# Kernel tuning notes

Measured on AMD Instinct MI355X. Metric: run time of the kernel, lower is better.

## Reference

```python
import jax, jax.numpy as jnp
import numpy as np

N = 50000  # nodes
E = 1600000  # edges
L = 2  # layers
D = 128  # input/hidden dim


def setup_inputs() -> dict:
    key = jax.random.key(0)
    ks = jax.random.split(key, 8)
    s = 1.0 / np.sqrt(D)
    return {
        "x": jax.random.normal(ks[0], (N, D), jnp.float32),
        "edge_index": jax.random.randint(ks[1], (2, E), 0, N, jnp.int64),
        "h": jax.random.normal(ks[2], (L, N, D), jnp.float32),
        "Wx": jax.random.normal(ks[3], (L, 3, D, D), jnp.float32) * s,
        "bx": jax.random.normal(ks[4], (L, 3, D), jnp.float32) * 0.01,
        "Wh": jax.random.normal(ks[5], (L, 3, D, D), jnp.float32) * s,
        "bh": jax.random.normal(ks[6], (L, 3, D), jnp.float32) * 0.01,
    }


def _gcn(x, W, b, src, dst, dinv):
    # GCNConv with added self-loops and symmetric normalization:
    # out = D^{-1/2} (A + I) D^{-1/2} X W + b
    hw = x @ W                                   # [N, H]
    norm = dinv[src] * dinv[dst]                 # [E]
    msg = hw[src] * norm[:, None]                # [E, H]
    agg = jax.ops.segment_sum(msg, dst, num_segments=N)
    agg = agg + hw * (dinv * dinv)[:, None]      # self-loop contribution
    return agg + b


def reference(x, edge_index, h, Wx, bx, Wh, bh):
    src = edge_index[0]
    dst = edge_index[1]
    # in-degree on destination nodes, including self-loop (+1)
    deg = jax.ops.segment_sum(jnp.ones((E,), x.dtype), dst, num_segments=N) + 1.0
    dinv = jax.lax.rsqrt(deg)

    outs = []
    inp = x
    for l in range(L):
        hl = h[l]
        z = jax.nn.sigmoid(_gcn(inp, Wx[l, 0], bx[l, 0], src, dst, dinv)
                           + _gcn(hl, Wh[l, 0], bh[l, 0], src, dst, dinv))
        r = jax.nn.sigmoid(_gcn(inp, Wx[l, 1], bx[l, 1], src, dst, dinv)
                           + _gcn(hl, Wh[l, 1], bh[l, 1], src, dst, dinv))
        h_tilde = jnp.tanh(_gcn(inp, Wx[l, 2], bx[l, 2], src, dst, dinv)
                           + _gcn(r * hl, Wh[l, 2], bh[l, 2], src, dst, dinv))
        out = z * hl + (1.0 - z) * h_tilde
        outs.append(out)
        inp = out
    return jnp.stack(outs, axis=0)  # [L, N, H]
```

## Files before the change

### kernel.cpp

```cpp
#include <hip/hip_runtime.h>

typedef __attribute__((ext_vector_type(8))) unsigned short us8;
typedef __attribute__((ext_vector_type(8))) short s8;
typedef __attribute__((ext_vector_type(4))) float f4;
typedef __attribute__((ext_vector_type(2))) float f2;

#define DEV static __device__ __forceinline__
#define CAP 128
#define NRG 128
#define NBB 256
#define SEGC 128

DEV float bf2f(unsigned short h){ return __uint_as_float(((unsigned)h)<<16); }
DEV unsigned short f2bf(float f){
  unsigned x = __float_as_uint(f);
  x += 0x7fffu + ((x>>16)&1u);
  return (unsigned short)(x>>16);
}
DEV float sigm(float x){ return 1.f/(1.f + __expf(-x)); }

__global__ __launch_bounds__(256) void k_bucket(const int* __restrict__ src,
    const int* __restrict__ dst, unsigned* __restrict__ buf,
    int* __restrict__ cnt2, int e, int n){
  __shared__ int lcnt[NRG];
  int b = blockIdx.x;
  for(int i=threadIdx.x;i<NRG;i+=256) lcnt[i] = 0;
  __syncthreads();
  int chunk = (e + NBB - 1)/NBB;
  int lo = b*chunk;
  int hi = lo + chunk; if(hi>e) hi=e;
  for(int i = lo + threadIdx.x; i < hi; i += 256){
    int d = dst[i], s = src[i];
    int r = (d*NRG)/n;
    int pos = atomicAdd(&lcnt[r], 1);
    if(pos < SEGC)
      buf[((size_t)r*NBB + b)*SEGC + pos] = ((unsigned)d<<16) | (unsigned)s;
  }
  __syncthreads();
  for(int i=threadIdx.x;i<NRG;i+=256) cnt2[i*NBB + b] = lcnt[i];
}

__global__ __launch_bounds__(256) void k_build2(const unsigned* __restrict__ buf,
    const int* __restrict__ cnt2, int* __restrict__ cnt,
    unsigned short* __restrict__ col, int n){
  int r = blockIdx.x;
  int lo = (r*n + NRG-1)/NRG;
  int hi = ((r+1)*n + NRG-1)/NRG;
  int span = hi - lo;
  __shared__ int lc[512];
  for(int i=threadIdx.x; i<span; i+=256) lc[i] = 0;
  __syncthreads();
  int lane = threadIdx.x & 63;
  for(int seg = threadIdx.x>>6; seg < NBB; seg += 4){
    int c = cnt2[r*NBB + seg]; if(c > SEGC) c = SEGC;
    const unsigned* p = buf + ((size_t)r*NBB + seg)*SEGC;
    for(int i = lane; i < c; i += 64){
      unsigned v = p[i];
      int d = (int)(v >> 16), s = (int)(v & 0xffffu);
      int slot = atomicAdd(&lc[d - lo], 1);
      col[(size_t)d*CAP + slot] = (unsigned short)s;
    }
  }
  __syncthreads();
  for(int i=threadIdx.x; i<span; i+=256) cnt[lo + i] = lc[i];
}

__global__ void k_setup(const int* __restrict__ cnt, float* __restrict__ dinv, int n,
                        const float* __restrict__ Wx, const float* __restrict__ Wh,
                        unsigned short* __restrict__ WT){
  int gN = (n + 255)/256;
  int b = blockIdx.x;
  if(b < gN){
    int i = b*256 + threadIdx.x;
    if(i<n) dinv[i] = rsqrtf((float)cnt[i] + 1.0f);
  } else {
    int i = (b-gN)*256 + threadIdx.x;
    int m = i >> 15;
    int rem = i & 32767;
    int j = rem >> 8;
    int k = rem & 255;
    float v = (k<128) ? Wx[((size_t)m*128 + k)*128 + j]
                      : Wh[((size_t)m*128 + (k-128))*128 + j];
    WT[(size_t)m*32768 + j*256 + k] = f2bf(v);
  }
}

template<int FULL>
__global__ void k_scale2(const float* __restrict__ inp, const float* __restrict__ hl,
                         const float* __restrict__ dinv, unsigned char* __restrict__ y2, int n){
  int i = blockIdx.x*blockDim.x+threadIdx.x;
  if(i >= n*32) return;
  int node = i>>5, d0 = (i&31)*4;
  float dv = dinv[node];
  f4 b = *(const f4*)(hl  + (size_t)node*128 + d0);
  unsigned pb = __builtin_amdgcn_cvt_pk_fp8_f32(dv*b[0], dv*b[1], 0, false);
  pb = __builtin_amdgcn_cvt_pk_fp8_f32(dv*b[2], dv*b[3], pb, true);
  *(unsigned*)(y2 + (size_t)node*256 + 128 + d0) = pb;
  if constexpr(FULL){
    f4 a = *(const f4*)(inp + (size_t)node*128 + d0);
    unsigned pa = __builtin_amdgcn_cvt_pk_fp8_f32(dv*a[0], dv*a[1], 0, false);
    pa = __builtin_amdgcn_cvt_pk_fp8_f32(dv*a[2], dv*a[3], pa, true);
    *(unsigned*)(y2 + (size_t)node*256 + d0) = pa;
  }
}

template<int DB>
__global__ __launch_bounds__(256) void k_agg(const unsigned char* __restrict__ y,
    const int* __restrict__ cnt, const unsigned short* __restrict__ col,
    const float* __restrict__ dinv, unsigned short* __restrict__ out0, int n)
{
  constexpr int GL = DB/16;
  constexpr int NG = 64/GL;
  constexpr int U = 8;
  int tid = threadIdx.x;
  int wave = tid>>6, lane = tid&63;
  int g = lane/GL, gl = lane%GL;
  int node = blockIdx.x*(4*NG) + wave*NG + g;
  if(node >= n) return;
  const unsigned char* yb = y + (size_t)gl*16;
  float acc[16];
  {
    uint4 q = *(const uint4*)(yb + (size_t)node*DB);
    const unsigned* qw = (const unsigned*)&q;
    #pragma unroll
    for(int w=0;w<4;++w){
      f2 lo = __builtin_amdgcn_cvt_pk_f32_fp8(qw[w], false);
      f2 hi = __builtin_amdgcn_cvt_pk_f32_fp8(qw[w], true);
      acc[w*4+0]=lo[0]; acc[w*4+1]=lo[1]; acc[w*4+2]=hi[0]; acc[w*4+3]=hi[1];
    }
  }
  const unsigned short* myrow = col + (size_t)node*CAP;
  int c_ = cnt[node];
  int last = c_ - 1;
  for(int i=0; i<c_; i += U){
    int s[U];
    #pragma unroll
    for(int u=0;u<U;++u){
      int ii = i + u; ii = (ii < last) ? ii : last;
      s[u] = myrow[ii];
    }
    uint4 v[U];
    #pragma unroll
    for(int u=0;u<U;++u) v[u] = *(const uint4*)(yb + (size_t)s[u]*DB);
    #pragma unroll
    for(int u=0;u<U;++u){
      if(i + u < c_){
        const unsigned* qw = (const unsigned*)&v[u];
        #pragma unroll
        for(int w=0;w<4;++w){
          f2 lo = __builtin_amdgcn_cvt_pk_f32_fp8(qw[w], false);
          f2 hi = __builtin_amdgcn_cvt_pk_f32_fp8(qw[w], true);
          acc[w*4+0]+=lo[0]; acc[w*4+1]+=lo[1]; acc[w*4+2]+=hi[0]; acc[w*4+3]+=hi[1];
        }
      }
    }
  }
  float dv = dinv[node];
  us8 w0, w1;
  #pragma unroll
  for(int j=0;j<8;++j){ w0[j]=f2bf(acc[j]*dv); w1[j]=f2bf(acc[8+j]*dv); }
  int c = gl*16;
  *(us8*)(out0 + (size_t)node*DB + c)     = w0;
  *(us8*)(out0 + (size_t)node*DB + c + 8) = w1;
}

template<int KB, int MODE>
__global__ __launch_bounds__(512) void k_gemm(
    const unsigned short* __restrict__ A, int astride,
    const unsigned short* __restrict__ Bsrc,
    const unsigned short* __restrict__ Zr, unsigned short* __restrict__ Zw,
    const float* __restrict__ hl, const float* __restrict__ dinv,
    const float* __restrict__ b1, const float* __restrict__ b2,
    const float* __restrict__ b3, const float* __restrict__ b4,
    unsigned char* __restrict__ yq, float* __restrict__ outp,
    unsigned char* __restrict__ y2out, int nrows)
{
  __shared__ unsigned char Bs[KB*256];
  const int t = threadIdx.x;
  constexpr int CPR = KB/8;
  for(int c = t; c < 128*CPR; c += 512){
    int j = c / CPR, kc = c % CPR;
    us8 v = *(const us8*)(Bsrc + (size_t)j*256 + kc*8);
    *(us8*)(Bs + ((j*(KB*2) + kc*16) ^ ((j&7)<<4))) = v;
  }
  __syncthreads();
  const int lane = t & 63, lo = lane & 15, hi = lane >> 4;
  const int r0 = blockIdx.x*128 + (t>>6)*16;
  const int arow = r0 + lo;
  const unsigned short* Ap = A + (size_t)(arow < nrows ? arow : 0)*astride + hi*8;
  f4 acc[8];
  #pragma unroll
  for(int n=0;n<8;++n) acc[n]=(f4)0.f;
  #pragma unroll
  for(int kk=0;kk<KB/32;++kk){
    s8 a = (arow<nrows) ? *(const s8*)(Ap + kk*32) : (s8)(short)0;
    #pragma unroll
    for(int n=0;n<8;++n){
      int j = n*16+lo;
      s8 b = *(const s8*)(Bs + ((j*(KB*2) + kk*64 + hi*16) ^ ((lo&7)<<4)));
      acc[n] = __builtin_amdgcn_mfma_f32_16x16x32_bf16(a, b, acc[n], 0,0,0);
    }
  }
  #pragma unroll
  for(int n=0;n<8;++n){
    const int colv = n*16 + lo;
    float bz = 0.f, bhv = 0.f;
    if constexpr(MODE==2){ bz = b1[colv] + b2[colv]; }
    if constexpr(MODE==3){ bz = b1[colv] + b2[colv]; bhv = b3[colv] + b4[colv]; }
    #pragma unroll
    for(int tt=0;tt<4;++tt){
      int row = r0 + hi*4 + tt;
      if(row >= nrows) continue;
      float v = acc[n][tt];
      if constexpr(MODE==0){
        Zw[(size_t)row*256 + colv] = f2bf(v);
      } else if constexpr(MODE==1){
        Zw[(size_t)row*256 + 128 + colv] = f2bf(v);
      } else if constexpr(MODE==2){
        float r = sigm(v + bz);
        float q = dinv[row] * r * hl[(size_t)row*128 + colv];
        unsigned pk = __builtin_amdgcn_cvt_pk_fp8_f32(q, q, 0, false);
        yq[(size_t)row*128 + colv] = (unsigned char)(pk & 0xff);
      } else {
        float z  = sigm(bf2f(Zr[(size_t)row*256 + colv]) + bz);
        float ht = tanhf(v + bf2f(Zr[(size_t)row*256 + 128 + colv]) + bhv);
        float ov = z*hl[(size_t)row*128 + colv] + (1.f - z)*ht;
        outp[(size_t)row*128 + colv] = ov;
        if(y2out){
          float q = dinv[row] * ov;
          unsigned pk = __builtin_amdgcn_cvt_pk_fp8_f32(q, q, 0, false);
          y2out[(size_t)row*256 + colv] = (unsigned char)(pk & 0xff);
        }
      }
    }
  }
}

extern "C" void kernel_launch(void* const* d_in, const int* in_sizes, int n_in,
                              void* d_out, int out_size, void* d_ws, size_t ws_size,
                              hipStream_t stream){
  const float* x  = (const float*)d_in[0];
  const int*   ei = (const int*)d_in[1];
  const float* h  = (const float*)d_in[2];
  const float* Wx = (const float*)d_in[3];
  const float* bx = (const float*)d_in[4];
  const float* Wh = (const float*)d_in[5];
  const float* bh = (const float*)d_in[6];
  float* out = (float*)d_out;

  const int N = in_sizes[0] / 128;
  const int E = in_sizes[1] / 2;
  const int L = in_sizes[2] / in_sizes[0];
  const int* src = ei;
  const int* dst = ei + E;

  char* w = (char*)d_ws;
  auto alloc = [&](size_t b)->char*{ char* p = w; w += (b + 255) & ~(size_t)255; return p; };
  int* cnt = (int*)alloc((size_t)N*sizeof(int));
  unsigned short* col = (unsigned short*)alloc((size_t)N*CAP*sizeof(short));
  float* dinv = (float*)alloc((size_t)N*sizeof(float));
  unsigned short* WT = (unsigned short*)alloc((size_t)6*32768*sizeof(short));
  unsigned char* y2 = (unsigned char*)alloc((size_t)N*256);
  unsigned short* axah = (unsigned short*)alloc((size_t)N*256*sizeof(short));
  unsigned char* yq = (unsigned char*)alloc((size_t)N*128);
  unsigned short* aq = (unsigned short*)alloc((size_t)N*128*sizeof(short));
  unsigned short* Zb = (unsigned short*)alloc((size_t)N*256*sizeof(short));
  unsigned* ebuf = (unsigned*)alloc((size_t)NRG*NBB*SEGC*sizeof(unsigned));
  int* cnt2 = (int*)alloc((size_t)NRG*NBB*sizeof(int));

  const int gN = (N + 255)/256;
  const int gew = (N*32 + 255)/256;
  const int g128 = (N + 127)/128;
  const int gagg4 = (N + 15)/16;
  const int gagg2 = (N + 31)/32;

  k_bucket<<<NBB,256,0,stream>>>(src, dst, ebuf, cnt2, E, N);
  k_build2<<<NRG,256,0,stream>>>(ebuf, cnt2, cnt, col, N);
  k_setup<<<gN + 768,256,0,stream>>>(cnt, dinv, N, Wx, Wh, WT);

  for(int l=0; l<L; ++l){
    const float* inp = (l==0) ? x : (out + (size_t)(l-1)*N*128);
    const float* hl  = h + (size_t)l*N*128;
    const float* bxz = bx + (size_t)(l*3+0)*128; const float* bhz = bh + (size_t)(l*3+0)*128;
    const float* bxr = bx + (size_t)(l*3+1)*128; const float* bhr = bh + (size_t)(l*3+1)*128;
    const float* bxh = bx + (size_t)(l*3+2)*128; const float* bhh = bh + (size_t)(l*3+2)*128;
    const unsigned short* Wz = WT + (size_t)(l*3+0)*32768;
    const unsigned short* Wr = WT + (size_t)(l*3+1)*32768;
    const unsigned short* Wh2= WT + (size_t)(l*3+2)*32768;

    if(l==0) k_scale2<1><<<gew,256,0,stream>>>(inp, hl, dinv, y2, N);
    else     k_scale2<0><<<gew,256,0,stream>>>(inp, hl, dinv, y2, N);
    k_agg<256><<<gagg4,256,0,stream>>>(y2, cnt, col, dinv, axah, N);
    k_gemm<256,0><<<g128,512,0,stream>>>(axah, 256, Wz, nullptr, Zb,
        nullptr, nullptr, nullptr, nullptr, nullptr, nullptr, nullptr, nullptr, nullptr, N);
    k_gemm<128,1><<<g128,512,0,stream>>>(axah, 256, Wh2, nullptr, Zb,
        nullptr, nullptr, nullptr, nullptr, nullptr, nullptr, nullptr, nullptr, nullptr, N);
    k_gemm<256,2><<<g128,512,0,stream>>>(axah, 256, Wr, nullptr, nullptr,
        hl, dinv, bxr, bhr, nullptr, nullptr, yq, nullptr, nullptr, N);
    k_agg<128><<<gagg2,256,0,stream>>>(yq, cnt, col, dinv, aq, N);
    k_gemm<128,3><<<g128,512,0,stream>>>(aq, 128, Wh2 + 128, Zb, nullptr,
        hl, dinv, bxz, bhz, bxh, bhh, nullptr, out + (size_t)l*N*128,
        (l+1<L) ? y2 : nullptr, N);
  }
}
```

Baseline: 407.8 us.

## Fuse gate GEMMs into two kernels and fold next-layer h scaling into epilogue

Merges the r-gate GEMM with the x-part of the candidate GEMM into one kernel, and moves the z-gate GEMM into the final combine kernel. The z pre-activation therefore no longer goes through a bf16 intermediate buffer. The final kernel also writes the dinv-scaled fp8 copy of the next layer's h, so the per-layer scale kernel only runs for layer 0. This cuts kernel launches and intermediate global traffic. In exchange it uses 64KB of shared memory per block and reloads B tiles sequentially, which may lower occupancy.

```diff
diff --git a/kernel.cpp b/kernel.cpp
--- a/kernel.cpp
+++ b/kernel.cpp
@@ -85,23 +85,20 @@
   }
 }
 
-template<int FULL>
 __global__ void k_scale2(const float* __restrict__ inp, const float* __restrict__ hl,
                          const float* __restrict__ dinv, unsigned char* __restrict__ y2, int n){
   int i = blockIdx.x*blockDim.x+threadIdx.x;
   if(i >= n*32) return;
   int node = i>>5, d0 = (i&31)*4;
   float dv = dinv[node];
+  f4 a = *(const f4*)(inp + (size_t)node*128 + d0);
   f4 b = *(const f4*)(hl  + (size_t)node*128 + d0);
+  unsigned pa = __builtin_amdgcn_cvt_pk_fp8_f32(dv*a[0], dv*a[1], 0, false);
+  pa = __builtin_amdgcn_cvt_pk_fp8_f32(dv*a[2], dv*a[3], pa, true);
   unsigned pb = __builtin_amdgcn_cvt_pk_fp8_f32(dv*b[0], dv*b[1], 0, false);
   pb = __builtin_amdgcn_cvt_pk_fp8_f32(dv*b[2], dv*b[3], pb, true);
+  *(unsigned*)(y2 + (size_t)node*256 + d0)       = pa;
   *(unsigned*)(y2 + (size_t)node*256 + 128 + d0) = pb;
-  if constexpr(FULL){
-    f4 a = *(const f4*)(inp + (size_t)node*128 + d0);
-    unsigned pa = __builtin_amdgcn_cvt_pk_fp8_f32(dv*a[0], dv*a[1], 0, false);
-    pa = __builtin_amdgcn_cvt_pk_fp8_f32(dv*a[2], dv*a[3], pa, true);
-    *(unsigned*)(y2 + (size_t)node*256 + d0) = pa;
-  }
 }
 
 template<int DB>
@@ -164,33 +161,22 @@
   *(us8*)(out0 + (size_t)node*DB + c + 8) = w1;
 }
 
-template<int KB, int MODE>
-__global__ __launch_bounds__(512) void k_gemm(
-    const unsigned short* __restrict__ A, int astride,
-    const unsigned short* __restrict__ Bsrc,
-    const unsigned short* __restrict__ Zr, unsigned short* __restrict__ Zw,
-    const float* __restrict__ hl, const float* __restrict__ dinv,
-    const float* __restrict__ b1, const float* __restrict__ b2,
-    const float* __restrict__ b3, const float* __restrict__ b4,
-    unsigned char* __restrict__ yq, float* __restrict__ outp,
-    unsigned char* __restrict__ y2out, int nrows)
-{
-  __shared__ unsigned char Bs[KB*256];
-  const int t = threadIdx.x;
+template<int KB>
+DEV void stageB512(unsigned char* Bs, const unsigned short* Bsrc, int srcStride,
+                   int srcOff, int t){
   constexpr int CPR = KB/8;
-  for(int c = t; c < 128*CPR; c += 512){
+  #pragma unroll
+  for(int i=0;i<128*CPR/512;++i){
+    int c = t + i*512;
     int j = c / CPR, kc = c % CPR;
-    us8 v = *(const us8*)(Bsrc + (size_t)j*256 + kc*8);
+    us8 v = *(const us8*)(Bsrc + (size_t)j*srcStride + srcOff + kc*8);
     *(us8*)(Bs + ((j*(KB*2) + kc*16) ^ ((j&7)<<4))) = v;
   }
-  __syncthreads();
-  const int lane = t & 63, lo = lane & 15, hi = lane >> 4;
-  const int r0 = blockIdx.x*128 + (t>>6)*16;
-  const int arow = r0 + lo;
+}
+template<int KB>
+DEV void mfmaK(const unsigned char* Bs, const unsigned short* A, int astride,
+               int arow, int nrows, int lo, int hi, f4 (&acc)[8]){
   const unsigned short* Ap = A + (size_t)(arow < nrows ? arow : 0)*astride + hi*8;
-  f4 acc[8];
-  #pragma unroll
-  for(int n=0;n<8;++n) acc[n]=(f4)0.f;
   #pragma unroll
   for(int kk=0;kk<KB/32;++kk){
     s8 a = (arow<nrows) ? *(const s8*)(Ap + kk*32) : (s8)(short)0;
@@ -201,36 +187,100 @@
       acc[n] = __builtin_amdgcn_mfma_f32_16x16x32_bf16(a, b, acc[n], 0,0,0);
     }
   }
+}
+
+__global__ __launch_bounds__(512) void k_gemmRH(
+    const unsigned short* __restrict__ axah, const unsigned short* __restrict__ Wr,
+    const unsigned short* __restrict__ Wh2, const float* __restrict__ hl,
+    const float* __restrict__ dinv, const float* __restrict__ bxr,
+    const float* __restrict__ bhr, unsigned char* __restrict__ yq,
+    unsigned short* __restrict__ Zbh, int nrows)
+{
+  __shared__ unsigned char Bs[65536];
+  const int t = threadIdx.x, lane = t & 63, lo = lane & 15, hi = lane >> 4;
+  const int r0 = blockIdx.x*128 + (t>>6)*16;
+  const int arow = r0 + lo;
+  f4 acc[8];
+  #pragma unroll
+  for(int n=0;n<8;++n) acc[n]=(f4)0.f;
+  stageB512<256>(Bs, Wr, 256, 0, t);
+  __syncthreads();
+  mfmaK<256>(Bs, axah, 256, arow, nrows, lo, hi, acc);
   #pragma unroll
   for(int n=0;n<8;++n){
     const int colv = n*16 + lo;
-    float bz = 0.f, bhv = 0.f;
-    if constexpr(MODE==2){ bz = b1[colv] + b2[colv]; }
-    if constexpr(MODE==3){ bz = b1[colv] + b2[colv]; bhv = b3[colv] + b4[colv]; }
+    float bz = bxr[colv] + bhr[colv];
+    #pragma unroll
+    for(int tt=0;tt<4;++tt){
+      int row = r0 + hi*4 + tt;
+      if(row < nrows){
+        float r = sigm(acc[n][tt] + bz);
+        float q = dinv[row] * r * hl[(size_t)row*128 + colv];
+        unsigned pk = __builtin_amdgcn_cvt_pk_fp8_f32(q, q, 0, false);
+        yq[(size_t)row*128 + colv] = (unsigned char)(pk & 0xff);
+      }
+    }
+  }
+  __syncthreads();
+  stageB512<128>(Bs, Wh2, 256, 0, t);
+  __syncthreads();
+  #pragma unroll
+  for(int n=0;n<8;++n) acc[n]=(f4)0.f;
+  mfmaK<128>(Bs, axah, 256, arow, nrows, lo, hi, acc);
+  #pragma unroll
+  for(int n=0;n<8;++n){
+    const int colv = n*16 + lo;
+    #pragma unroll
+    for(int tt=0;tt<4;++tt){
+      int row = r0 + hi*4 + tt;
+      if(row < nrows) Zbh[(size_t)row*128 + colv] = f2bf(acc[n][tt]);
+    }
+  }
+}
+
+__global__ __launch_bounds__(512) void k_gemmZF(
+    const unsigned short* __restrict__ axah, const unsigned short* __restrict__ aq,
+    const unsigned short* __restrict__ Wz, const unsigned short* __restrict__ Wh2,
+    const unsigned short* __restrict__ Zbh, const float* __restrict__ hl,
+    const float* __restrict__ hnext, const float* __restrict__ dinv,
+    const float* __restrict__ bxz, const float* __restrict__ bhz,
+    const float* __restrict__ bxh, const float* __restrict__ bhh,
+    float* __restrict__ outp, unsigned char* __restrict__ y2out, int nrows)
+{
+  __shared__ unsigned char Bs[65536];
+  const int t = threadIdx.x, lane = t & 63, lo = lane & 15, hi = lane >> 4;
+  const int r0 = blockIdx.x*128 + (t>>6)*16;
+  const int arow = r0 + lo;
+  f4 accZ[8], accH[8];
+  #pragma unroll
+  for(int n=0;n<8;++n){ accZ[n]=(f4)0.f; accH[n]=(f4)0.f; }
+  stageB512<256>(Bs, Wz, 256, 0, t);
+  __syncthreads();
+  mfmaK<256>(Bs, axah, 256, arow, nrows, lo, hi, accZ);
+  __syncthreads();
+  stageB512<128>(Bs, Wh2, 256, 128, t);
+  __syncthreads();
+  mfmaK<128>(Bs, aq, 128, arow, nrows, lo, hi, accH);
+  #pragma unroll
+  for(int n=0;n<8;++n){
+    const int colv = n*16 + lo;
+    float bz = bxz[colv] + bhz[colv];
+    float bh = bxh[colv] + bhh[colv];
     #pragma unroll
     for(int tt=0;tt<4;++tt){
       int row = r0 + hi*4 + tt;
       if(row >= nrows) continue;
-      float v = acc[n][tt];
-      if constexpr(MODE==0){
-        Zw[(size_t)row*256 + colv] = f2bf(v);
-      } else if constexpr(MODE==1){
-        Zw[(size_t)row*256 + 128 + colv] = f2bf(v);
-      } else if constexpr(MODE==2){
-        float r = sigm(v + bz);
-        float q = dinv[row] * r * hl[(size_t)row*128 + colv];
-        unsigned pk = __builtin_amdgcn_cvt_pk_fp8_f32(q, q, 0, false);
-        yq[(size_t)row*128 + colv] = (unsigned char)(pk & 0xff);
-      } else {
-        float z  = sigm(bf2f(Zr[(size_t)row*256 + colv]) + bz);
-        float ht = tanhf(v + bf2f(Zr[(size_t)row*256 + 128 + colv]) + bhv);
-        float ov = z*hl[(size_t)row*128 + colv] + (1.f - z)*ht;
-        outp[(size_t)row*128 + colv] = ov;
-        if(y2out){
-          float q = dinv[row] * ov;
-          unsigned pk = __builtin_amdgcn_cvt_pk_fp8_f32(q, q, 0, false);
-          y2out[(size_t)row*256 + colv] = (unsigned char)(pk & 0xff);
-        }
+      float z  = sigm(accZ[n][tt] + bz);
+      float ht = tanhf(accH[n][tt] + bf2f(Zbh[(size_t)row*128 + colv]) + bh);
+      float ov = z*hl[(size_t)row*128 + colv] + (1.f - z)*ht;
+      outp[(size_t)row*128 + colv] = ov;
+      if(y2out){
+        float dv = dinv[row];
+        unsigned pk = __builtin_amdgcn_cvt_pk_fp8_f32(dv*ov, dv*ov, 0, false);
+        y2out[(size_t)row*256 + colv] = (unsigned char)(pk & 0xff);
+        float hv = dv * hnext[(size_t)row*128 + colv];
+        unsigned ph = __builtin_amdgcn_cvt_pk_fp8_f32(hv, hv, 0, false);
+        y2out[(size_t)row*256 + 128 + colv] = (unsigned char)(ph & 0xff);
       }
     }
   }
@@ -264,7 +314,7 @@
   unsigned short* axah = (unsigned short*)alloc((size_t)N*256*sizeof(short));
   unsigned char* yq = (unsigned char*)alloc((size_t)N*128);
   unsigned short* aq = (unsigned short*)alloc((size_t)N*128*sizeof(short));
-  unsigned short* Zb = (unsigned short*)alloc((size_t)N*256*sizeof(short));
+  unsigned short* Zbh = (unsigned short*)alloc((size_t)N*128*sizeof(short));
   unsigned* ebuf = (unsigned*)alloc((size_t)NRG*NBB*SEGC*sizeof(unsigned));
   int* cnt2 = (int*)alloc((size_t)NRG*NBB*sizeof(int));
 
@@ -279,7 +329,6 @@
   k_setup<<<gN + 768,256,0,stream>>>(cnt, dinv, N, Wx, Wh, WT);
 
   for(int l=0; l<L; ++l){
-    const float* inp = (l==0) ? x : (out + (size_t)(l-1)*N*128);
     const float* hl  = h + (size_t)l*N*128;
     const float* bxz = bx + (size_t)(l*3+0)*128; const float* bhz = bh + (size_t)(l*3+0)*128;
     const float* bxr = bx + (size_t)(l*3+1)*128; const float* bhr = bh + (size_t)(l*3+1)*128;
@@ -288,18 +337,13 @@
     const unsigned short* Wr = WT + (size_t)(l*3+1)*32768;
     const unsigned short* Wh2= WT + (size_t)(l*3+2)*32768;
 
-    if(l==0) k_scale2<1><<<gew,256,0,stream>>>(inp, hl, dinv, y2, N);
-    else     k_scale2<0><<<gew,256,0,stream>>>(inp, hl, dinv, y2, N);
+    if(l==0) k_scale2<<<gew,256,0,stream>>>(x, hl, dinv, y2, N);
     k_agg<256><<<gagg4,256,0,stream>>>(y2, cnt, col, dinv, axah, N);
-    k_gemm<256,0><<<g128,512,0,stream>>>(axah, 256, Wz, nullptr, Zb,
-        nullptr, nullptr, nullptr, nullptr, nullptr, nullptr, nullptr, nullptr, nullptr, N);
-    k_gemm<128,1><<<g128,512,0,stream>>>(axah, 256, Wh2, nullptr, Zb,
-        nullptr, nullptr, nullptr, nullptr, nullptr, nullptr, nullptr, nullptr, nullptr, N);
-    k_gemm<256,2><<<g128,512,0,stream>>>(axah, 256, Wr, nullptr, nullptr,
-        hl, dinv, bxr, bhr, nullptr, nullptr, yq, nullptr, nullptr, N);
+    k_gemmRH<<<g128,512,0,stream>>>(axah, Wr, Wh2, hl, dinv, bxr, bhr, yq, Zbh, N);
     k_agg<128><<<gagg2,256,0,stream>>>(yq, cnt, col, dinv, aq, N);
-    k_gemm<128,3><<<g128,512,0,stream>>>(aq, 128, Wh2 + 128, Zb, nullptr,
-        hl, dinv, bxz, bhz, bxh, bhh, nullptr, out + (size_t)l*N*128,
+    k_gemmZF<<<g128,512,0,stream>>>(axah, aq, Wz, Wh2, Zbh, hl,
+        (l+1<L) ? (h + (size_t)(l+1)*N*128) : nullptr, dinv,
+        bxz, bhz, bxh, bhh, out + (size_t)l*N*128,
         (l+1<L) ? y2 : nullptr, N);
   }
 }
```

After: 382.1 us. 1.07x faster.
